# Performance work log

Measured on AMD Instinct MI355X. Metric: run time of the kernel, lower is better.

Reference implementation:

```python
import jax, jax.numpy as jnp
import numpy as np

EPS_ATTN = 1e-6
EPS_LN = 1e-5

def _layernorm(x, g, b):
    mu = jnp.mean(x, axis=-1, keepdims=True)
    var = jnp.mean(jnp.square(x - mu), axis=-1, keepdims=True)
    return (x - mu) * jax.lax.rsqrt(var + EPS_LN) * g + b

def _phi(x):
    return jax.nn.elu(x) + 1.0

def setup_inputs() -> dict:
    key = jax.random.key(0)
    ks = jax.random.split(key, 7)
    N, L, C = 4, 16384, 256
    s = 1.0 / np.sqrt(C)
    return {
        "x": jax.random.normal(ks[0], (N, L, C), dtype=jnp.float32),
        "Wq": jax.random.normal(ks[1], (C, C), dtype=jnp.float32) * s,
        "Wk": jax.random.normal(ks[2], (C, C), dtype=jnp.float32) * s,
        "Wv": jax.random.normal(ks[3], (C, C), dtype=jnp.float32) * s,
        "Wm": jax.random.normal(ks[4], (C, C), dtype=jnp.float32) * s,
        "W1": jax.random.normal(ks[5], (2 * C, C), dtype=jnp.float32) * (1.0 / np.sqrt(2 * C)),
        "W2": jax.random.normal(ks[6], (C, C), dtype=jnp.float32) * s,
        "g1": jnp.ones((C,), jnp.float32),
        "b1": jnp.zeros((C,), jnp.float32),
        "g2": jnp.ones((C,), jnp.float32),
        "b2": jnp.zeros((C,), jnp.float32),
    }

def reference(x, Wq, Wk, Wv, Wm, W1, W2, g1, b1, g2, b2):
    N, L, C = x.shape
    H = 8
    D = C // H
    # qkv projections -> [n, l, h, d]
    q = (x @ Wq).reshape(N, L, H, D)
    k = (x @ Wk).reshape(N, L, H, D)
    v = (x @ Wv).reshape(N, L, H, D)
    # linear attention (elu feature map)
    Q = _phi(q)
    K = _phi(k)
    v_scaled = v / L
    KV = jnp.einsum('nshd,nshv->nhdv', K, v_scaled)          # [n,h,d,d]
    Z = 1.0 / (jnp.einsum('nlhd,nhd->nlh', Q, K.sum(axis=1)) + EPS_ATTN)
    msg = jnp.einsum('nlhd,nhdv,nlh->nlhv', Q, KV, Z) * L    # [n,l,h,d]
    # merge + norm1
    msg = msg.reshape(N, L, C) @ Wm
    msg = _layernorm(msg, g1, b1)
    # mlp(cat[x, msg]) + norm2
    h = jax.nn.relu(jnp.concatenate([x, msg], axis=-1) @ W1)
    msg = _layernorm(h @ W2, g2, b2)
    return x + msg
```

## Files before the change

kernel.cpp:

```cpp
#include <hip/hip_runtime.h>
#include <hip/hip_bf16.h>
#include <math.h>

#define NB 4
#define LB 16384
#define CB 256
#define HB 8
#define DB 32
#define NLB (NB * LB)
#define SPLITS 32
#define SPLIT_ROWS (LB / SPLITS)

typedef unsigned short ushort_t;
typedef __attribute__((ext_vector_type(8))) short bf16x8;
typedef __attribute__((ext_vector_type(4))) float f32x4;

__device__ __forceinline__ ushort_t f2b(float f) {
  union { __hip_bfloat16 h; ushort_t u; } cv;
  cv.h = __float2bfloat16(f);
  return cv.u;
}
__device__ __forceinline__ float b2f(ushort_t u) {
  union { __hip_bfloat16 h; ushort_t u; } cv;
  cv.u = u;
  return __bfloat162float(cv.h);
}

__device__ __forceinline__ void gload16(const void* g, void* l) {
  __builtin_amdgcn_global_load_lds(
      (const __attribute__((address_space(1))) void*)g,
      (__attribute__((address_space(3))) void*)l, 16, 0, 0);
}

template <int AF32>
__device__ __forceinline__ void gemm_core3(const void* A, int strideA,
                                           const ushort_t* __restrict__ WT,
                                           int strideB, short* As, short* Bs,
                                           f32x4 acc[4][4], int nk) {
  const int t = threadIdx.x;
  const int lane = t & 63;
  const int w = t >> 6, wr = w >> 2, wc = w & 3;
  const int q = lane >> 4, lr = lane & 15;
  for (int ks = 0; ks < nk; ++ks) {
    const int k0 = ks * 64;
    __syncthreads();
    if (AF32) {
      #pragma unroll
      for (int rep = 0; rep < 2; ++rep) {
        int si = t + 512 * rep;
        int r = si >> 3, s = si & 7;
        int dst = r * 64 + ((s ^ (r & 7)) << 3);
        const float* src = (const float*)A + (size_t)r * strideA + k0 + 8 * s;
        float4 fa = *(const float4*)src;
        float4 fb = *(const float4*)(src + 4);
        ushort_t tmp[8] = {f2b(fa.x), f2b(fa.y), f2b(fa.z), f2b(fa.w),
                           f2b(fb.x), f2b(fb.y), f2b(fb.z), f2b(fb.w)};
        *(uint4*)&As[dst] = *(const uint4*)tmp;
      }
    } else {
      #pragma unroll
      for (int rep = 0; rep < 2; ++rep) {
        int chunk = w * 2 + rep;
        int si = chunk * 64 + lane;
        int r = si >> 3, s = si & 7;
        const ushort_t* src =
            (const ushort_t*)A + (size_t)r * strideA + k0 + 8 * (s ^ (r & 7));
        gload16(src, As + chunk * 512);
      }
    }
    #pragma unroll
    for (int rep = 0; rep < 4; ++rep) {
      int chunk = w * 4 + rep;
      int si = chunk * 64 + lane;
      int r = si >> 3, s = si & 7;
      const ushort_t* src = WT + (size_t)r * strideB + k0 + 8 * (s ^ (r & 7));
      gload16(src, Bs + chunk * 512);
    }
    __syncthreads();
    #pragma unroll
    for (int kk = 0; kk < 2; ++kk) {
      bf16x8 af[4], bfr[4];
      const int s = 4 * kk + q;
      #pragma unroll
      for (int m = 0; m < 4; ++m) {
        int r = wr * 64 + 16 * m + lr;
        af[m] = *(const bf16x8*)&As[r * 64 + ((s ^ (r & 7)) << 3)];
      }
      #pragma unroll
      for (int nn = 0; nn < 4; ++nn) {
        int c = wc * 64 + 16 * nn + lr;
        bfr[nn] = *(const bf16x8*)&Bs[c * 64 + ((s ^ (c & 7)) << 3)];
      }
      #pragma unroll
      for (int m = 0; m < 4; ++m)
        #pragma unroll
        for (int nn = 0; nn < 4; ++nn)
          acc[m][nn] = __builtin_amdgcn_mfma_f32_16x16x32_bf16(
              af[m], bfr[nn], acc[m][nn], 0, 0, 0);
    }
  }
}

__device__ __forceinline__ void zero_acc(f32x4 acc[4][4]) {
  #pragma unroll
  for (int m = 0; m < 4; ++m)
    #pragma unroll
    for (int n = 0; n < 4; ++n) acc[m][n] = 0.0f;
}

__device__ __forceinline__ void store_bf16(f32x4 acc[4][4], ushort_t* out,
                                           int row0, int do_phi) {
  const int t = threadIdx.x;
  const int lane = t & 63, w = t >> 6, wr = w >> 2, wc = w & 3;
  const int q = lane >> 4, lr = lane & 15;
  #pragma unroll
  for (int m = 0; m < 4; ++m)
    #pragma unroll
    for (int nn = 0; nn < 4; ++nn) {
      int col = wc * 64 + 16 * nn + lr;
      #pragma unroll
      for (int reg = 0; reg < 4; ++reg) {
        int row = row0 + wr * 64 + 16 * m + 4 * q + reg;
        float v = acc[m][nn][reg];
        if (do_phi) v = (v > 0.f) ? v + 1.f : __expf(v);
        out[(size_t)row * 256 + col] = f2b(v);
      }
    }
}

__global__ __launch_bounds__(256) void xconv_kernel(const float* __restrict__ x,
                                                    ushort_t* __restrict__ xb) {
  size_t i = ((size_t)blockIdx.x * 256 + threadIdx.x) * 8;
  float4 a = *(const float4*)&x[i];
  float4 b = *(const float4*)&x[i + 4];
  ushort_t tmp[8] = {f2b(a.x), f2b(a.y), f2b(a.z), f2b(a.w),
                     f2b(b.x), f2b(b.y), f2b(b.z), f2b(b.w)};
  *(uint4*)&xb[i] = *(const uint4*)tmp;
}

__global__ __launch_bounds__(512) void qkv3_kernel(
    ushort_t* __restrict__ xb, const ushort_t* __restrict__ WqT,
    const ushort_t* __restrict__ WkT, const ushort_t* __restrict__ WvT,
    ushort_t* __restrict__ Qb, ushort_t* __restrict__ Kb) {
  __shared__ short As[128 * 64];
  __shared__ short Bs[256 * 64];
  const int row0 = blockIdx.x * 128;
  const ushort_t* Ax = xb + (size_t)row0 * 256;
  f32x4 acc[4][4];

  zero_acc(acc);
  gemm_core3<0>(Ax, 256, WqT, 256, As, Bs, acc, 4);
  store_bf16(acc, Qb, row0, 1);
  zero_acc(acc);
  gemm_core3<0>(Ax, 256, WkT, 256, As, Bs, acc, 4);
  store_bf16(acc, Kb, row0, 1);
  zero_acc(acc);
  gemm_core3<0>(Ax, 256, WvT, 256, As, Bs, acc, 4);
  __syncthreads();
  store_bf16(acc, xb, row0, 0);
}

template <int RESID>
__global__ __launch_bounds__(512) void gemmln2(
    const ushort_t* __restrict__ A, const ushort_t* __restrict__ WT,
    const float* __restrict__ g, const float* __restrict__ bvec,
    const float* __restrict__ resid, void* Out) {
  __shared__ short As[128 * 64];
  __shared__ short Bs[256 * 64];
  __shared__ float p1[128][4], p2[128][4], mus[128], rns[128];
  const int row0 = blockIdx.x * 128;
  f32x4 acc[4][4];
  zero_acc(acc);
  gemm_core3<0>(A + (size_t)row0 * 256, 256, WT, 256, As, Bs, acc, 4);
  const int t = threadIdx.x;
  const int lane = t & 63, w = t >> 6, wr = w >> 2, wc = w & 3;
  const int q = lane >> 4, lr = lane & 15;
  #pragma unroll
  for (int m = 0; m < 4; ++m)
    #pragma unroll
    for (int reg = 0; reg < 4; ++reg) {
      float s1 = 0.f, s2 = 0.f;
      #pragma unroll
      for (int nn = 0; nn < 4; ++nn) {
        float v = acc[m][nn][reg];
        s1 += v;
        s2 += v * v;
      }
      #pragma unroll
      for (int msk = 8; msk >= 1; msk >>= 1) {
        s1 += __shfl_xor(s1, msk);
        s2 += __shfl_xor(s2, msk);
      }
      if (lr == 0) {
        int rl = wr * 64 + 16 * m + 4 * q + reg;
        p1[rl][wc] = s1;
        p2[rl][wc] = s2;
      }
    }
  __syncthreads();
  if (t < 128) {
    float a = 0.f, b = 0.f;
    #pragma unroll
    for (int ww = 0; ww < 4; ++ww) {
      a += p1[t][ww];
      b += p2[t][ww];
    }
    float mu = a * (1.f / 256.f);
    float var = b * (1.f / 256.f) - mu * mu;
    mus[t] = mu;
    rns[t] = rsqrtf(var + 1e-5f);
  }
  __syncthreads();
  #pragma unroll
  for (int m = 0; m < 4; ++m)
    #pragma unroll
    for (int nn = 0; nn < 4; ++nn) {
      int col = wc * 64 + 16 * nn + lr;
      float gv = g[col], bv = bvec[col];
      #pragma unroll
      for (int reg = 0; reg < 4; ++reg) {
        int rl = wr * 64 + 16 * m + 4 * q + reg;
        int row = row0 + rl;
        float v = (acc[m][nn][reg] - mus[rl]) * rns[rl] * gv + bv;
        if (RESID) {
          v += resid[(size_t)row * 256 + col];
          ((float*)Out)[(size_t)row * 256 + col] = v;
        } else {
          ((ushort_t*)Out)[(size_t)row * 256 + col] = f2b(v);
        }
      }
    }
}

__global__ __launch_bounds__(512) void mlp1_v2(const float* __restrict__ x,
                                               const ushort_t* __restrict__ m1,
                                               const ushort_t* __restrict__ W1T,
                                               ushort_t* __restrict__ H) {
  __shared__ short As[128 * 64];
  __shared__ short Bs[256 * 64];
  const int row0 = blockIdx.x * 128;
  f32x4 acc[4][4];
  zero_acc(acc);
  gemm_core3<1>(x + (size_t)row0 * 256, 256, W1T, 512, As, Bs, acc, 4);
  gemm_core3<0>(m1 + (size_t)row0 * 256, 256, W1T + 256, 512, As, Bs, acc, 4);
  const int t = threadIdx.x;
  const int lane = t & 63, w = t >> 6, wr = w >> 2, wc = w & 3;
  const int q = lane >> 4, lr = lane & 15;
  #pragma unroll
  for (int m = 0; m < 4; ++m)
    #pragma unroll
    for (int nn = 0; nn < 4; ++nn) {
      int col = wc * 64 + 16 * nn + lr;
      #pragma unroll
      for (int reg = 0; reg < 4; ++reg) {
        int row = row0 + wr * 64 + 16 * m + 4 * q + reg;
        H[(size_t)row * 256 + col] = f2b(fmaxf(acc[m][nn][reg], 0.f));
      }
    }
}

__global__ __launch_bounds__(256) void wtrans_kernel(const float* __restrict__ W,
                                                     ushort_t* __restrict__ WT,
                                                     int K, int N) {
  __shared__ float tile[64][65];
  const int t = threadIdx.x;
  const int bx = blockIdx.x, by = blockIdx.y;
  for (int i = t; i < 4096; i += 256) {
    int r = i >> 6, c = i & 63;
    tile[r][c] = W[(size_t)(by * 64 + r) * N + bx * 64 + c];
  }
  __syncthreads();
  for (int i = t; i < 4096; i += 256) {
    int r = i >> 6, c = i & 63;
    WT[(size_t)(bx * 64 + r) * K + by * 64 + c] = f2b(tile[c][r]);
  }
}

__global__ __launch_bounds__(256) void kv_partial_kernel(
    const ushort_t* __restrict__ K, const ushort_t* __restrict__ V,
    float* __restrict__ Pp) {
  __shared__ float Ksh[64][32];
  __shared__ float Vsh[64][32];
  const int nh = blockIdx.x;
  const int n = nh >> 3, h = nh & 7;
  const int l0 = n * LB + blockIdx.y * SPLIT_ROWS;
  const int t = threadIdx.x;
  const int d = t >> 3, vg = t & 7;
  float acc[4] = {0.f, 0.f, 0.f, 0.f};
  float ksacc = 0.f;
  for (int tile = 0; tile < SPLIT_ROWS / 64; ++tile) {
    __syncthreads();
    {
      int rr = t >> 2, c8 = t & 3;
      size_t base = (size_t)(l0 + tile * 64 + rr) * 256 + h * 32 + 8 * c8;
      uint4 kr = *(const uint4*)&K[base];
      uint4 vr = *(const uint4*)&V[base];
      const ushort_t* kp = (const ushort_t*)&kr;
      const ushort_t* vp = (const ushort_t*)&vr;
      #pragma unroll
      for (int e = 0; e < 8; ++e) {
        Ksh[rr][8 * c8 + e] = b2f(kp[e]);
        Vsh[rr][8 * c8 + e] = b2f(vp[e]);
      }
    }
    __syncthreads();
    for (int r = 0; r < 64; ++r) {
      float kv = Ksh[r][d];
      if (vg == 0) ksacc += kv;
      #pragma unroll
      for (int qq = 0; qq < 4; ++qq)
        acc[qq] = fmaf(kv, Vsh[r][vg * 4 + qq], acc[qq]);
    }
  }
  float* rec = Pp + (size_t)(blockIdx.y * (NB * HB) + nh) * 1056;
  #pragma unroll
  for (int qq = 0; qq < 4; ++qq) rec[d * 32 + vg * 4 + qq] = acc[qq];
  if (vg == 0) rec[1024 + d] = ksacc;
}

__global__ __launch_bounds__(256) void kv_final_kernel(
    const float* __restrict__ Pp, float* __restrict__ KV,
    float* __restrict__ KS) {
  const int nh = blockIdx.x;
  const int t = threadIdx.x;
  for (int i = t; i < 1056; i += 256) {
    float s = 0.f;
    for (int sp = 0; sp < SPLITS; ++sp)
      s += Pp[(size_t)(sp * (NB * HB) + nh) * 1056 + i];
    if (i < 1024)
      KV[(size_t)nh * 1024 + i] = s;
    else
      KS[nh * 32 + (i - 1024)] = s;
  }
}

__global__ __launch_bounds__(256) void msg_kernel(ushort_t* __restrict__ QM,
                                                  const float* __restrict__ KV,
                                                  const float* __restrict__ KS) {
  __shared__ float Qs[32][256];
  __shared__ float kvs[8][32][32];
  __shared__ float ks[8][32];
  __shared__ float zs[32][8];
  const int t = threadIdx.x;
  const int row0 = blockIdx.x * 32;
  const int n = row0 >> 14;
  #pragma unroll
  for (int j = 0; j < 4; ++j) {
    int fi = t + 256 * j;
    int rr = fi >> 5, g8 = fi & 31;
    uint4 raw = *(const uint4*)&QM[(size_t)(row0 + rr) * 256 + 8 * g8];
    const ushort_t* pr = (const ushort_t*)&raw;
    #pragma unroll
    for (int e = 0; e < 8; ++e) Qs[rr][8 * g8 + e] = b2f(pr[e]);
  }
  const float* KVn = KV + (size_t)n * (HB * DB * DB);
  #pragma unroll
  for (int r = 0; r < 8; ++r) {
    int fi = t + 256 * r;
    ((float4*)kvs)[fi] = ((const float4*)KVn)[fi];
  }
  ((float*)ks)[t] = KS[n * 256 + t];
  __syncthreads();
  {
    int l = t >> 3, h = t & 7;
    float dsum = 0.f;
    #pragma unroll
    for (int dd = 0; dd < 32; ++dd)
      dsum = fmaf(Qs[l][h * 32 + dd], ks[h][dd], dsum);
    zs[l][h] = 1.0f / (dsum + 1e-6f);
  }
  __syncthreads();
  const int c = t, h = c >> 5, v = c & 31;
  for (int l = 0; l < 32; ++l) {
    float s = 0.f;
    #pragma unroll
    for (int dd = 0; dd < 32; ++dd)
      s = fmaf(Qs[l][h * 32 + dd], kvs[h][dd][v], s);
    QM[(size_t)(row0 + l) * 256 + c] = f2b(s * zs[l][h]);
  }
}

extern "C" void kernel_launch(void* const* d_in, const int* in_sizes, int n_in,
                              void* d_out, int out_size, void* d_ws,
                              size_t ws_size, hipStream_t stream) {
  const float* x = (const float*)d_in[0];
  const float* Wq = (const float*)d_in[1];
  const float* Wk = (const float*)d_in[2];
  const float* Wv = (const float*)d_in[3];
  const float* Wm = (const float*)d_in[4];
  const float* W1 = (const float*)d_in[5];
  const float* W2 = (const float*)d_in[6];
  const float* g1 = (const float*)d_in[7];
  const float* b1 = (const float*)d_in[8];
  const float* g2 = (const float*)d_in[9];
  const float* b2 = (const float*)d_in[10];
  float* out = (float*)d_out;

  const size_t PE = (size_t)NLB * CB;
  ushort_t* Qb = (ushort_t*)d_out;
  ushort_t* Kb = (ushort_t*)((char*)d_out + PE * 2);

  char* wsb = (char*)d_ws;
  ushort_t* Vxb = (ushort_t*)wsb;
  float* Pp = (float*)(wsb + PE * 2);
  float* KVb = Pp + (size_t)SPLITS * NB * HB * 1056;
  float* KSb = KVb + (size_t)NB * HB * DB * DB;
  ushort_t* WqT = (ushort_t*)(KSb + NB * HB * DB);
  ushort_t* WkT = WqT + 256 * 256;
  ushort_t* WvT = WkT + 256 * 256;
  ushort_t* WmT = WvT + 256 * 256;
  ushort_t* W2T = WmT + 256 * 256;
  ushort_t* W1T = W2T + 256 * 256;

  wtrans_kernel<<<dim3(4, 4), 256, 0, stream>>>(Wq, WqT, 256, 256);
  wtrans_kernel<<<dim3(4, 4), 256, 0, stream>>>(Wk, WkT, 256, 256);
  wtrans_kernel<<<dim3(4, 4), 256, 0, stream>>>(Wv, WvT, 256, 256);
  wtrans_kernel<<<dim3(4, 4), 256, 0, stream>>>(Wm, WmT, 256, 256);
  wtrans_kernel<<<dim3(4, 4), 256, 0, stream>>>(W2, W2T, 256, 256);
  wtrans_kernel<<<dim3(4, 8), 256, 0, stream>>>(W1, W1T, 512, 256);

  xconv_kernel<<<PE / 2048, 256, 0, stream>>>(x, Vxb);
  qkv3_kernel<<<NLB / 128, 512, 0, stream>>>(Vxb, WqT, WkT, WvT, Qb, Kb);
  kv_partial_kernel<<<dim3(NB * HB, SPLITS), 256, 0, stream>>>(Kb, Vxb, Pp);
  kv_final_kernel<<<NB * HB, 256, 0, stream>>>(Pp, KVb, KSb);
  msg_kernel<<<NLB / 32, 256, 0, stream>>>(Qb, KVb, KSb);
  gemmln2<0><<<NLB / 128, 512, 0, stream>>>(Qb, WmT, g1, b1, nullptr, Kb);
  mlp1_v2<<<NLB / 128, 512, 0, stream>>>(x, Kb, W1T, Vxb);
  gemmln2<1><<<NLB / 128, 512, 0, stream>>>(Vxb, W2T, g2, b2, x, out);
}
```

Baseline: 395.2 us.

## Fold KV state into merge weight and replace msg kernel with row scaling

Precomputes, per batch, a combined matrix M = blockdiag(KV_h) @ Wm in bf16, so the merge GEMM consumes Z-scaled Q directly. The per-row KV matmul kernel becomes a lightweight kernel that only applies the normaliser Z to Q in place. The six weight-transpose launches are also merged into one launch. This removes a full pass of per-row 32x32 matmuls at the cost of a small per-batch matrix product. It adds an extra bf16 rounding of the combined weights, and the merge GEMM now reads a per-batch weight matrix.

```diff
diff --git a/kernel.cpp b/kernel.cpp
--- a/kernel.cpp
+++ b/kernel.cpp
@@ -169,9 +169,10 @@
   __shared__ short Bs[256 * 64];
   __shared__ float p1[128][4], p2[128][4], mus[128], rns[128];
   const int row0 = blockIdx.x * 128;
+  const ushort_t* WTn = RESID ? WT : WT + (size_t)(row0 >> 14) * 65536;
   f32x4 acc[4][4];
   zero_acc(acc);
-  gemm_core3<0>(A + (size_t)row0 * 256, 256, WT, 256, As, Bs, acc, 4);
+  gemm_core3<0>(A + (size_t)row0 * 256, 256, WTn, 256, As, Bs, acc, 4);
   const int t = threadIdx.x;
   const int lane = t & 63, w = t >> 6, wr = w >> 2, wc = w & 3;
   const int q = lane >> 4, lr = lane & 15;
@@ -259,15 +260,31 @@
     }
 }
 
-__global__ __launch_bounds__(256) void wtrans_kernel(const float* __restrict__ W,
-                                                     ushort_t* __restrict__ WT,
-                                                     int K, int N) {
+__global__ __launch_bounds__(256) void wtrans_all(
+    const float* __restrict__ Wq, const float* __restrict__ Wk,
+    const float* __restrict__ Wv, const float* __restrict__ W2,
+    const float* __restrict__ W1, ushort_t* __restrict__ WqT,
+    ushort_t* __restrict__ WkT, ushort_t* __restrict__ WvT,
+    ushort_t* __restrict__ W2T, ushort_t* __restrict__ W1T) {
+  const int z = blockIdx.z;
+  const float* W;
+  ushort_t* WT;
+  int K = 256;
+  switch (z) {
+    case 0: W = Wq; WT = WqT; break;
+    case 1: W = Wk; WT = WkT; break;
+    case 2: W = Wv; WT = WvT; break;
+    case 3: W = W2; WT = W2T; break;
+    default: W = W1; WT = W1T; K = 512; break;
+  }
+  const int by = blockIdx.y;
+  if (by * 64 >= K) return;
   __shared__ float tile[64][65];
   const int t = threadIdx.x;
-  const int bx = blockIdx.x, by = blockIdx.y;
+  const int bx = blockIdx.x;
   for (int i = t; i < 4096; i += 256) {
     int r = i >> 6, c = i & 63;
-    tile[r][c] = W[(size_t)(by * 64 + r) * N + bx * 64 + c];
+    tile[r][c] = W[(size_t)(by * 64 + r) * 256 + bx * 64 + c];
   }
   __syncthreads();
   for (int i = t; i < 4096; i += 256) {
@@ -318,66 +335,63 @@
   if (vg == 0) rec[1024 + d] = ksacc;
 }
 
-__global__ __launch_bounds__(256) void kv_final_kernel(
-    const float* __restrict__ Pp, float* __restrict__ KV,
-    float* __restrict__ KS) {
+__global__ __launch_bounds__(256) void kv_finalM_kernel(
+    const float* __restrict__ Pp, const float* __restrict__ Wm,
+    ushort_t* __restrict__ MT, float* __restrict__ KS) {
   const int nh = blockIdx.x;
-  const int t = threadIdx.x;
+  const int n = nh >> 3, h = nh & 7;
+  const int t = threadIdx.x;
+  __shared__ float kvs[1024];
   for (int i = t; i < 1056; i += 256) {
     float s = 0.f;
     for (int sp = 0; sp < SPLITS; ++sp)
       s += Pp[(size_t)(sp * (NB * HB) + nh) * 1056 + i];
     if (i < 1024)
-      KV[(size_t)nh * 1024 + i] = s;
+      kvs[i] = s;
     else
-      KS[nh * 32 + (i - 1024)] = s;
-  }
-}
-
-__global__ __launch_bounds__(256) void msg_kernel(ushort_t* __restrict__ QM,
-                                                  const float* __restrict__ KV,
-                                                  const float* __restrict__ KS) {
-  __shared__ float Qs[32][256];
-  __shared__ float kvs[8][32][32];
-  __shared__ float ks[8][32];
-  __shared__ float zs[32][8];
+      KS[n * 256 + h * 32 + (i - 1024)] = s;
+  }
+  __syncthreads();
+  float wmv[32];
+  #pragma unroll
+  for (int v = 0; v < 32; ++v) wmv[v] = Wm[(size_t)(32 * h + v) * 256 + t];
+  ushort_t mrow[32];
+  #pragma unroll
+  for (int d = 0; d < 32; ++d) {
+    float s = 0.f;
+    #pragma unroll
+    for (int v = 0; v < 32; ++v) s = fmaf(kvs[d * 32 + v], wmv[v], s);
+    mrow[d] = f2b(s);
+  }
+  ushort_t* dst = MT + (size_t)n * 65536 + (size_t)t * 256 + 32 * h;
+  #pragma unroll
+  for (int j = 0; j < 4; ++j)
+    *(uint4*)&dst[8 * j] = *(const uint4*)&mrow[8 * j];
+}
+
+__global__ __launch_bounds__(256) void zscale_kernel(ushort_t* __restrict__ Q,
+                                                     const float* __restrict__ KS) {
+  __shared__ float ks[256];
   const int t = threadIdx.x;
   const int row0 = blockIdx.x * 32;
   const int n = row0 >> 14;
-  #pragma unroll
-  for (int j = 0; j < 4; ++j) {
-    int fi = t + 256 * j;
-    int rr = fi >> 5, g8 = fi & 31;
-    uint4 raw = *(const uint4*)&QM[(size_t)(row0 + rr) * 256 + 8 * g8];
-    const ushort_t* pr = (const ushort_t*)&raw;
-    #pragma unroll
-    for (int e = 0; e < 8; ++e) Qs[rr][8 * g8 + e] = b2f(pr[e]);
-  }
-  const float* KVn = KV + (size_t)n * (HB * DB * DB);
-  #pragma unroll
-  for (int r = 0; r < 8; ++r) {
-    int fi = t + 256 * r;
-    ((float4*)kvs)[fi] = ((const float4*)KVn)[fi];
-  }
-  ((float*)ks)[t] = KS[n * 256 + t];
-  __syncthreads();
-  {
-    int l = t >> 3, h = t & 7;
-    float dsum = 0.f;
-    #pragma unroll
-    for (int dd = 0; dd < 32; ++dd)
-      dsum = fmaf(Qs[l][h * 32 + dd], ks[h][dd], dsum);
-    zs[l][h] = 1.0f / (dsum + 1e-6f);
-  }
-  __syncthreads();
-  const int c = t, h = c >> 5, v = c & 31;
-  for (int l = 0; l < 32; ++l) {
-    float s = 0.f;
-    #pragma unroll
-    for (int dd = 0; dd < 32; ++dd)
-      s = fmaf(Qs[l][h * 32 + dd], kvs[h][dd][v], s);
-    QM[(size_t)(row0 + l) * 256 + c] = f2b(s * zs[l][h]);
-  }
+  ks[t] = KS[(n << 8) + t];
+  __syncthreads();
+  const int r = t >> 3, h = t & 7;
+  ushort_t* p = Q + (size_t)(row0 + r) * 256 + 32 * h;
+  uint4 raw[4];
+  #pragma unroll
+  for (int j = 0; j < 4; ++j) raw[j] = *(const uint4*)&p[8 * j];
+  const ushort_t* q16 = (const ushort_t*)raw;
+  float dot = 0.f;
+  #pragma unroll
+  for (int d = 0; d < 32; ++d) dot = fmaf(b2f(q16[d]), ks[32 * h + d], dot);
+  const float z = 1.0f / (dot + 1e-6f);
+  ushort_t outv[32];
+  #pragma unroll
+  for (int d = 0; d < 32; ++d) outv[d] = f2b(b2f(q16[d]) * z);
+  #pragma unroll
+  for (int j = 0; j < 4; ++j) *(uint4*)&p[8 * j] = *(const uint4*)&outv[8 * j];
 }
 
 extern "C" void kernel_launch(void* const* d_in, const int* in_sizes, int n_in,
@@ -403,28 +417,22 @@
   char* wsb = (char*)d_ws;
   ushort_t* Vxb = (ushort_t*)wsb;
   float* Pp = (float*)(wsb + PE * 2);
-  float* KVb = Pp + (size_t)SPLITS * NB * HB * 1056;
-  float* KSb = KVb + (size_t)NB * HB * DB * DB;
-  ushort_t* WqT = (ushort_t*)(KSb + NB * HB * DB);
+  float* KSb = Pp + (size_t)SPLITS * NB * HB * 1056;
+  ushort_t* MT = (ushort_t*)(KSb + NB * HB * DB);
+  ushort_t* WqT = MT + (size_t)NB * 256 * 256;
   ushort_t* WkT = WqT + 256 * 256;
   ushort_t* WvT = WkT + 256 * 256;
-  ushort_t* WmT = WvT + 256 * 256;
-  ushort_t* W2T = WmT + 256 * 256;
+  ushort_t* W2T = WvT + 256 * 256;
   ushort_t* W1T = W2T + 256 * 256;
 
-  wtrans_kernel<<<dim3(4, 4), 256, 0, stream>>>(Wq, WqT, 256, 256);
-  wtrans_kernel<<<dim3(4, 4), 256, 0, stream>>>(Wk, WkT, 256, 256);
-  wtrans_kernel<<<dim3(4, 4), 256, 0, stream>>>(Wv, WvT, 256, 256);
-  wtrans_kernel<<<dim3(4, 4), 256, 0, stream>>>(Wm, WmT, 256, 256);
-  wtrans_kernel<<<dim3(4, 4), 256, 0, stream>>>(W2, W2T, 256, 256);
-  wtrans_kernel<<<dim3(4, 8), 256, 0, stream>>>(W1, W1T, 512, 256);
-
+  wtrans_all<<<dim3(4, 8, 5), 256, 0, stream>>>(Wq, Wk, Wv, W2, W1, WqT, WkT,
+                                                WvT, W2T, W1T);
   xconv_kernel<<<PE / 2048, 256, 0, stream>>>(x, Vxb);
   qkv3_kernel<<<NLB / 128, 512, 0, stream>>>(Vxb, WqT, WkT, WvT, Qb, Kb);
   kv_partial_kernel<<<dim3(NB * HB, SPLITS), 256, 0, stream>>>(Kb, Vxb, Pp);
-  kv_final_kernel<<<NB * HB, 256, 0, stream>>>(Pp, KVb, KSb);
-  msg_kernel<<<NLB / 32, 256, 0, stream>>>(Qb, KVb, KSb);
-  gemmln2<0><<<NLB / 128, 512, 0, stream>>>(Qb, WmT, g1, b1, nullptr, Kb);
+  kv_finalM_kernel<<<NB * HB, 256, 0, stream>>>(Pp, Wm, MT, KSb);
+  zscale_kernel<<<NLB / 32, 256, 0, stream>>>(Qb, KSb);
+  gemmln2<0><<<NLB / 128, 512, 0, stream>>>(Qb, MT, g1, b1, nullptr, Kb);
   mlp1_v2<<<NLB / 128, 512, 0, stream>>>(x, Kb, W1T, Vxb);
   gemmln2<1><<<NLB / 128, 512, 0, stream>>>(Vxb, W2T, g2, b2, x, out);
 }
```

After: 366.1 us. 7.4% less time.
